# Optimization experiments

Measured on AMD Instinct MI355X. Metric: run time of the kernel, lower is better.

The kernel has to match this reference:

```python
import jax, jax.numpy as jnp
import numpy as np

BLOCK = 8
HALO = 3
HEADS = 8
DIM_HEAD = 64
DIM = 128
MAX_NEG = -3.402823466e38  # -torch.finfo(float32).max, matches the CUDA kernel


def _extract_patches(xp, nh, nw, block, K):
    # xp: [b, c, Hp, Wp] (already padded). Returns [b, c, nh, nw, K, K]
    ih = (jnp.arange(nh) * block)[:, None] + jnp.arange(K)[None, :]  # [nh, K]
    iw = (jnp.arange(nw) * block)[:, None] + jnp.arange(K)[None, :]  # [nw, K]
    return xp[..., ih[:, None, :, None], iw[None, :, None, :]]


def setup_inputs() -> dict:
    key = jax.random.key(0)
    k1, k2, k3, k4, k5 = jax.random.split(key, 5)
    inner = HEADS * DIM_HEAD
    x = jax.random.normal(k1, (4, DIM, 128, 128), dtype=jnp.float32)
    s = 1.0 / np.sqrt(DIM)
    Wq = jax.random.normal(k2, (DIM, inner), dtype=jnp.float32) * s
    Wkv = jax.random.normal(k3, (DIM, 2 * inner), dtype=jnp.float32) * s
    Wo = jax.random.normal(k4, (inner, DIM), dtype=jnp.float32) * (1.0 / np.sqrt(inner))
    bo = jax.random.normal(k5, (DIM,), dtype=jnp.float32) * 0.01
    return {"x": x, "Wq": Wq, "Wkv": Wkv, "Wo": Wo, "bo": bo}


def reference(x, Wq, Wkv, Wo, bo):
    b, c, h, w = x.shape
    block, halo, heads, dh = BLOCK, HALO, HEADS, DIM_HEAD
    K = block + 2 * halo
    nh, nw = h // block, w // block
    nb = nh * nw
    I, J = block * block, K * K
    scale = dh ** -0.5

    # queries per block: [b, nb, I, c]
    q_inp = (x.reshape(b, c, nh, block, nw, block)
              .transpose(0, 2, 4, 3, 5, 1)
              .reshape(b, nb, I, c))

    # halo key/value windows via unfold-equivalent patch extraction
    xp = jnp.pad(x, ((0, 0), (0, 0), (halo, halo), (halo, halo)))
    kv = _extract_patches(xp, nh, nw, block, K)           # [b, c, nh, nw, K, K]
    kv_inp = kv.transpose(0, 2, 3, 4, 5, 1).reshape(b, nb, J, c)

    # mask: True where the halo window overlaps padding
    ones = jnp.pad(jnp.ones((1, 1, h, w), x.dtype),
                   ((0, 0), (0, 0), (halo, halo), (halo, halo)))
    mask = (_extract_patches(ones, nh, nw, block, K).reshape(nb, J) == 0)

    q = (q_inp @ Wq).reshape(b, nb, I, heads, dh) * scale
    kvp = kv_inp @ Wkv                                    # [b, nb, J, 2*inner]
    inner = heads * dh
    k = kvp[..., :inner].reshape(b, nb, J, heads, dh)
    v = kvp[..., inner:].reshape(b, nb, J, heads, dh)

    sim = jnp.einsum('bnihd,bnjhd->bnhij', q, k)          # [b, nb, heads, I, J]
    sim = jnp.where(mask[None, :, None, None, :], MAX_NEG, sim)
    attn = jax.nn.softmax(sim, axis=-1)
    out = jnp.einsum('bnhij,bnjhd->bnihd', attn, v)       # [b, nb, I, heads, dh]

    out = out.reshape(b, nb, I, inner) @ Wo + bo          # [b, nb, I, c]
    out = (out.reshape(b, nh, nw, block, block, c)
              .transpose(0, 5, 1, 3, 2, 4)
              .reshape(b, c, h, w))
    return out
```

## Files before the change

kernel.cpp:

```cpp
#include <hip/hip_runtime.h>
#include <hip/hip_bf16.h>

typedef unsigned short ushort_t;
typedef __attribute__((ext_vector_type(8))) short short8;
typedef __attribute__((ext_vector_type(4))) short short4v;
typedef __attribute__((ext_vector_type(4))) float float4v;

__device__ __forceinline__ unsigned short f2b(float f) {
    unsigned int u = __float_as_uint(f);
    return (unsigned short)((u + 0x7fffu + ((u >> 16) & 1u)) >> 16);
}

#define MFMA(a, b, c) __builtin_amdgcn_mfma_f32_16x16x32_bf16((a), (b), (c), 0, 0, 0)

__global__ void prep_weights(const float* __restrict__ Wq,
                             const float* __restrict__ Wkv,
                             const float* __restrict__ Wo,
                             ushort_t* __restrict__ ws)
{
    int t = blockIdx.x * 256 + threadIdx.x;
    if (t < 65536) {
        int n = t >> 7, c = t & 127;
        ws[t] = f2b(Wq[c * 512 + n]);
    } else if (t < 196608) {
        int u = t - 65536;
        int h = u >> 14, r = (u >> 7) & 127, c = u & 127;
        float v = (r < 64) ? Wkv[c * 1024 + h * 64 + r]
                           : Wkv[c * 1024 + 512 + h * 64 + (r - 64)];
        ws[t] = f2b(v);
    } else {
        int u = t - 196608;
        int c = u >> 9, n = u & 511;
        ws[t] = f2b(Wo[n * 128 + c]);
    }
}

__global__ __launch_bounds__(512, 2)
void halo_attn_mfma(const float* __restrict__ xg,
                    const ushort_t* __restrict__ wqt,
                    const ushort_t* __restrict__ wkvt,
                    const ushort_t* __restrict__ wot,
                    const float* __restrict__ bo,
                    float* __restrict__ outg)
{
    extern __shared__ char smem[];
    ushort_t* s_x   = (ushort_t*)(smem);
    ushort_t* k_s   = (ushort_t*)(smem + 56576);
    ushort_t* v_t   = (ushort_t*)(smem + 86528);
    ushort_t* p_s   = (ushort_t*)(smem + 116224);
    ushort_t* q_s   = (ushort_t*)(smem + 145920);
    float*    s_max = (float*)(smem + 155136);
    float*    s_sum = (float*)(smem + 155648);
    ushort_t* o_s   = k_s;

    const int tid  = threadIdx.x;
    const int w    = tid >> 6;
    const int lane = tid & 63;
    const int m    = lane & 15;
    const int quad = lane >> 4;

    const int wg  = blockIdx.x;
    const int b   = wg >> 8;
    const int blk = wg & 255;
    const int by = blk >> 4, bx = blk & 15;
    const int y0 = by * 8 - 3, x0 = bx * 8 - 3;

    for (int t = tid; t < 64 * 24; t += 512) {
        int r = t / 24, c = 208 + (t - r * 24);
        p_s[r * 232 + c] = 0;
        v_t[r * 232 + c] = 0;
    }
    for (int t = tid; t < 128 * 256; t += 512) {
        int c = t >> 8, wy = (t >> 4) & 15, wx = t & 15;
        if (wy < 14 && wx < 14) {
            int gy = y0 + wy, gx = x0 + wx;
            float v = 0.f;
            if ((unsigned)gy < 128u && (unsigned)gx < 128u)
                v = xg[((b * 128 + c) * 128 + gy) * 128 + gx];
            s_x[(wy * 14 + wx) * 136 + c] = f2b(v);
        }
    }
    for (int t = tid; t < 12 * 128; t += 512)
        s_x[(196 + (t >> 7)) * 136 + (t & 127)] = 0;
    __syncthreads();

    float4v res[4];
#pragma unroll
    for (int i = 0; i < 4; ++i) res[i] = (float4v){0.f, 0.f, 0.f, 0.f};

    for (int h = 0; h < 8; ++h) {
        {
            const int nt = w & 7;
            const ushort_t* bb = wkvt + h * 16384 + (nt * 16 + m) * 128 + quad * 8;
            short8 bfr[4];
#pragma unroll
            for (int kk = 0; kk < 4; ++kk) bfr[kk] = *(const short8*)(bb + kk * 32);
#pragma unroll 1
            for (int jt = 0; jt < 13; ++jt) {
                float4v c = {0.f, 0.f, 0.f, 0.f};
                const ushort_t* ar = s_x + (jt * 16 + m) * 136 + quad * 8;
#pragma unroll
                for (int kk = 0; kk < 4; ++kk) {
                    short8 af = *(const short8*)(ar + kk * 32);
                    c = MFMA(af, bfr[kk], c);
                }
                if (nt < 4) {
                    int d = nt * 16 + m;
#pragma unroll
                    for (int r = 0; r < 4; ++r)
                        k_s[(jt * 16 + quad * 4 + r) * 72 + d] = f2b(c[r]);
                } else {
                    int dv = (nt - 4) * 16 + m;
                    short4v pk;
#pragma unroll
                    for (int r = 0; r < 4; ++r) pk[r] = (short)f2b(c[r]);
                    *(short4v*)(v_t + dv * 232 + jt * 16 + quad * 4) = pk;
                }
            }
        }
        {
            const int nt = w & 3;
            const ushort_t* bb = wqt + (h * 64 + nt * 16 + m) * 128 + quad * 8;
            short8 bfr[4];
#pragma unroll
            for (int kk = 0; kk < 4; ++kk) bfr[kk] = *(const short8*)(bb + kk * 32);
#pragma unroll
            for (int tt = 0; tt < 2; ++tt) {
                int it = (w >> 2) + tt * 2;
                float4v c = {0.f, 0.f, 0.f, 0.f};
                int i = it * 16 + m;
                int jq = ((i >> 3) + 3) * 14 + (i & 7) + 3;
                const ushort_t* ar = s_x + jq * 136 + quad * 8;
#pragma unroll
                for (int kk = 0; kk < 4; ++kk) {
                    short8 af = *(const short8*)(ar + kk * 32);
                    c = MFMA(af, bfr[kk], c);
                }
                int d = nt * 16 + m;
#pragma unroll
                for (int r = 0; r < 4; ++r)
                    q_s[(it * 16 + quad * 4 + r) * 72 + d] = f2b(c[r] * 0.125f);
            }
        }
        __syncthreads();

        {
            const int it = w & 3;
            const int half = w >> 2;
            const int jt0 = half ? 7 : 0;
            const int ntile = half ? 6 : 7;
            short8 aq[2];
#pragma unroll
            for (int kk = 0; kk < 2; ++kk)
                aq[kk] = *(const short8*)(q_s + (it * 16 + m) * 72 + kk * 32 + quad * 8);
            float sc[7][4];
            int okm = 0;
            float pm[4] = {-3.0e38f, -3.0e38f, -3.0e38f, -3.0e38f};
#pragma unroll
            for (int u = 0; u < 7; ++u) {
                if (u < ntile) {
                    int jt = jt0 + u;
                    float4v c = {0.f, 0.f, 0.f, 0.f};
#pragma unroll
                    for (int kk = 0; kk < 2; ++kk) {
                        short8 bk = *(const short8*)(k_s + (jt * 16 + m) * 72 + kk * 32 + quad * 8);
                        c = MFMA(aq[kk], bk, c);
                    }
                    int j = jt * 16 + m;
                    bool ok = false;
                    if (j < 196) {
                        int wy = j / 14, wx = j - wy * 14;
                        ok = ((unsigned)(y0 + wy) < 128u) && ((unsigned)(x0 + wx) < 128u);
                    }
                    if (ok) {
                        okm |= (1 << u);
#pragma unroll
                        for (int r = 0; r < 4; ++r) pm[r] = fmaxf(pm[r], c[r]);
                    }
#pragma unroll
                    for (int r = 0; r < 4; ++r) sc[u][r] = c[r];
                }
            }
#pragma unroll
            for (int mk = 1; mk < 16; mk <<= 1)
#pragma unroll
                for (int r = 0; r < 4; ++r)
                    pm[r] = fmaxf(pm[r], __shfl_xor(pm[r], mk, 64));
            if (m == 0) {
#pragma unroll
                for (int r = 0; r < 4; ++r)
                    s_max[half * 64 + it * 16 + quad * 4 + r] = pm[r];
            }
            __syncthreads();
            float m0[4], sm[4];
#pragma unroll
            for (int r = 0; r < 4; ++r) {
                int i = it * 16 + quad * 4 + r;
                m0[r] = fmaxf(s_max[i], s_max[64 + i]);
                sm[r] = 0.f;
            }
#pragma unroll
            for (int u = 0; u < 7; ++u) {
                if (u < ntile) {
                    int j = (jt0 + u) * 16 + m;
                    bool ok = (okm >> u) & 1;
#pragma unroll
                    for (int r = 0; r < 4; ++r) {
                        float p = ok ? __expf(sc[u][r] - m0[r]) : 0.f;
                        sm[r] += p;
                        p_s[(it * 16 + quad * 4 + r) * 232 + j] = f2b(p);
                    }
                }
            }
#pragma unroll
            for (int mk = 1; mk < 16; mk <<= 1)
#pragma unroll
                for (int r = 0; r < 4; ++r)
                    sm[r] += __shfl_xor(sm[r], mk, 64);
            if (m == 0) {
#pragma unroll
                for (int r = 0; r < 4; ++r)
                    s_sum[half * 64 + it * 16 + quad * 4 + r] = sm[r];
            }
            __syncthreads();
        }

        {
            const int nt = w & 3;
#pragma unroll
            for (int tt = 0; tt < 2; ++tt) {
                int it = (w >> 2) + tt * 2;
                float4v c = {0.f, 0.f, 0.f, 0.f};
                const ushort_t* ar = p_s + (it * 16 + m) * 232 + quad * 8;
                const ushort_t* br = v_t + (nt * 16 + m) * 232 + quad * 8;
#pragma unroll
                for (int kk = 0; kk < 7; ++kk) {
                    short8 af = *(const short8*)(ar + kk * 32);
                    short8 bf = *(const short8*)(br + kk * 32);
                    c = MFMA(af, bf, c);
                }
#pragma unroll
                for (int r = 0; r < 4; ++r) {
                    int i = it * 16 + quad * 4 + r;
                    float rv = 1.f / (s_sum[i] + s_sum[64 + i]);
                    o_s[i * 72 + nt * 16 + m] = f2b(c[r] * rv);
                }
            }
        }
        __syncthreads();

        {
            const int ct = w & 7;
            const ushort_t* bb = wot + (ct * 16 + m) * 512 + h * 64 + quad * 8;
            short8 bw[2];
#pragma unroll
            for (int kk = 0; kk < 2; ++kk) bw[kk] = *(const short8*)(bb + kk * 32);
#pragma unroll
            for (int it = 0; it < 4; ++it) {
                float4v c = res[it];
                const ushort_t* ar = o_s + (it * 16 + m) * 72 + quad * 8;
#pragma unroll
                for (int kk = 0; kk < 2; ++kk) {
                    short8 af = *(const short8*)(ar + kk * 32);
                    c = MFMA(af, bw[kk], c);
                }
                res[it] = c;
            }
        }
        __syncthreads();
    }

    {
        const int cch = (w & 7) * 16 + m;
        const float bias = bo[cch];
#pragma unroll
        for (int it = 0; it < 4; ++it) {
#pragma unroll
            for (int r = 0; r < 4; ++r) {
                int i = it * 16 + quad * 4 + r;
                int gy = by * 8 + (i >> 3), gx = bx * 8 + (i & 7);
                outg[((b * 128 + cch) * 128 + gy) * 128 + gx] = res[it][r] + bias;
            }
        }
    }
}

extern "C" void kernel_launch(void* const* d_in, const int* in_sizes, int n_in,
                              void* d_out, int out_size, void* d_ws, size_t ws_size,
                              hipStream_t stream) {
    const float* x   = (const float*)d_in[0];
    const float* Wq  = (const float*)d_in[1];
    const float* Wkv = (const float*)d_in[2];
    const float* Wo  = (const float*)d_in[3];
    const float* bo  = (const float*)d_in[4];
    float* out = (float*)d_out;
    ushort_t* ws = (ushort_t*)d_ws;

    prep_weights<<<dim3(1024), dim3(256), 0, stream>>>(Wq, Wkv, Wo, ws);

    (void)hipFuncSetAttribute((const void*)halo_attn_mfma,
                              hipFuncAttributeMaxDynamicSharedMemorySize, 156160);
    halo_attn_mfma<<<dim3(1024), dim3(512), 156160, stream>>>(
        x, ws, ws + 65536, ws + 196608, bo, out);
}
```

Before: 422.7 us.

## Swizzle LDS layouts, keep x fragments in registers, alias x buffer to shrink LDS

Replaces the padded LDS layouts with XOR-swizzled 16-byte chunk layouts for x, K, V, P, Q and O. The x window fragments for K/V and Q projections are now loaded once into registers, so the x buffer can alias K/V storage. This cuts dynamic shared memory from about 156KB to about 101KB. Each wave now loops over all 8 column tiles for its row tiles instead of one tile over all rows. It also vectorizes the x staging load into 8-channel packs. The aim is fewer bank conflicts and lower LDS pressure, at the cost of more registers held across the head loop.

```diff
diff --git a/kernel.cpp b/kernel.cpp
--- a/kernel.cpp
+++ b/kernel.cpp
@@ -44,14 +44,14 @@
                     float* __restrict__ outg)
 {
     extern __shared__ char smem[];
-    ushort_t* s_x   = (ushort_t*)(smem);
-    ushort_t* k_s   = (ushort_t*)(smem + 56576);
-    ushort_t* v_t   = (ushort_t*)(smem + 86528);
-    ushort_t* p_s   = (ushort_t*)(smem + 116224);
-    ushort_t* q_s   = (ushort_t*)(smem + 145920);
-    float*    s_max = (float*)(smem + 155136);
-    float*    s_sum = (float*)(smem + 155648);
-    ushort_t* o_s   = k_s;
+    ushort_t* k_u   = (ushort_t*)(smem);
+    ushort_t* v_u   = (ushort_t*)(smem + 26624);
+    ushort_t* sx_u  = (ushort_t*)(smem);
+    ushort_t* p_u   = (ushort_t*)(smem + 59392);
+    ushort_t* q_u   = (ushort_t*)(smem + 92160);
+    float*    s_max = (float*)(smem + 100352);
+    float*    s_sum = (float*)(smem + 100864);
+    ushort_t* o_u   = k_u;
 
     const int tid  = threadIdx.x;
     const int w    = tid >> 6;
@@ -65,81 +65,118 @@
     const int by = blk >> 4, bx = blk & 15;
     const int y0 = by * 8 - 3, x0 = bx * 8 - 3;
 
-    for (int t = tid; t < 64 * 24; t += 512) {
-        int r = t / 24, c = 208 + (t - r * 24);
-        p_s[r * 232 + c] = 0;
-        v_t[r * 232 + c] = 0;
-    }
-    for (int t = tid; t < 128 * 256; t += 512) {
-        int c = t >> 8, wy = (t >> 4) & 15, wx = t & 15;
-        if (wy < 14 && wx < 14) {
-            int gy = y0 + wy, gx = x0 + wx;
-            float v = 0.f;
-            if ((unsigned)gy < 128u && (unsigned)gx < 128u)
-                v = xg[((b * 128 + c) * 128 + gy) * 128 + gx];
-            s_x[(wy * 14 + wx) * 136 + c] = f2b(v);
-        }
-    }
-    for (int t = tid; t < 12 * 128; t += 512)
-        s_x[(196 + (t >> 7)) * 136 + (t & 127)] = 0;
+    const short8 zero8 = {0, 0, 0, 0, 0, 0, 0, 0};
+
+    for (int job = tid; job < 3136; job += 512) {
+        int cc  = job / 196;
+        int pos = job - cc * 196;
+        int wy = pos / 14;
+        int wx = pos - wy * 14;
+        int gy = y0 + wy, gx = x0 + wx;
+        short8 pk = zero8;
+        if ((unsigned)gy < 128u && (unsigned)gx < 128u) {
+            const float* xp = xg + ((b * 128 + cc * 8) * 128 + gy) * 128 + gx;
+#pragma unroll
+            for (int r = 0; r < 8; ++r)
+                pk[r] = (short)f2b(xp[r * 16384]);
+        }
+        *(short8*)(sx_u + pos * 128 + ((cc ^ (pos & 7)) << 3)) = pk;
+    }
+    for (int t = tid; t < 192; t += 512) {
+        int row = 196 + (t >> 4), cc = t & 15;
+        *(short8*)(sx_u + row * 128 + ((cc ^ (row & 7)) << 3)) = zero8;
+    }
     __syncthreads();
 
+    short8 xa[2][4];
+#pragma unroll
+    for (int u = 0; u < 2; ++u) {
+        int jt = w + 8 * u;
+#pragma unroll
+        for (int kk = 0; kk < 4; ++kk) {
+            xa[u][kk] = zero8;
+            if (jt < 13) {
+                int row = jt * 16 + m;
+                xa[u][kk] = *(const short8*)(sx_u + row * 128 +
+                                             (((kk * 4 + quad) ^ (m & 7)) << 3));
+            }
+        }
+    }
+    short8 qa[2][4];
+#pragma unroll
+    for (int tt = 0; tt < 2; ++tt) {
+        int it = (w >> 2) + 2 * tt;
+        int i  = it * 16 + m;
+        int jq = ((i >> 3) + 3) * 14 + (i & 7) + 3;
+#pragma unroll
+        for (int kk = 0; kk < 4; ++kk)
+            qa[tt][kk] = *(const short8*)(sx_u + jq * 128 +
+                                          (((kk * 4 + quad) ^ (jq & 7)) << 3));
+    }
+    __syncthreads();
+
+    for (int t = tid; t < 256; t += 512) {
+        int row = t >> 2, cc = 26 + (t & 1);
+        ushort_t* base = ((t >> 1) & 1) ? v_u : p_u;
+        *(short8*)(base + row * 256 + ((cc ^ (row & 7)) << 3)) = zero8;
+    }
+
     float4v res[4];
 #pragma unroll
     for (int i = 0; i < 4; ++i) res[i] = (float4v){0.f, 0.f, 0.f, 0.f};
 
     for (int h = 0; h < 8; ++h) {
-        {
-            const int nt = w & 7;
+#pragma unroll 1
+        for (int nt = 0; nt < 8; ++nt) {
             const ushort_t* bb = wkvt + h * 16384 + (nt * 16 + m) * 128 + quad * 8;
             short8 bfr[4];
 #pragma unroll
             for (int kk = 0; kk < 4; ++kk) bfr[kk] = *(const short8*)(bb + kk * 32);
-#pragma unroll 1
-            for (int jt = 0; jt < 13; ++jt) {
+#pragma unroll
+            for (int u = 0; u < 2; ++u) {
+                int jt = w + 8 * u;
+                if (jt < 13) {
+                    float4v c = {0.f, 0.f, 0.f, 0.f};
+#pragma unroll
+                    for (int kk = 0; kk < 4; ++kk) c = MFMA(xa[u][kk], bfr[kk], c);
+                    if (nt < 4) {
+                        int chunkx = nt * 2 + (m >> 3), inner = m & 7;
+#pragma unroll
+                        for (int r = 0; r < 4; ++r) {
+                            int row = jt * 16 + quad * 4 + r;
+                            k_u[row * 64 + ((chunkx ^ (row & 7)) << 3) + inner] = f2b(c[r]);
+                        }
+                    } else {
+                        int dv = (nt - 4) * 16 + m;
+                        int chunk = jt * 2 + (quad >> 1);
+                        short4v pk;
+#pragma unroll
+                        for (int r = 0; r < 4; ++r) pk[r] = (short)f2b(c[r]);
+                        *(short4v*)(v_u + dv * 256 + ((chunk ^ (dv & 7)) << 3) +
+                                    (quad & 1) * 4) = pk;
+                    }
+                }
+            }
+        }
+        {
+            const int ntq = w & 3;
+            const ushort_t* bb = wqt + (h * 64 + ntq * 16 + m) * 128 + quad * 8;
+            short8 bfr[4];
+#pragma unroll
+            for (int kk = 0; kk < 4; ++kk) bfr[kk] = *(const short8*)(bb + kk * 32);
+#pragma unroll
+            for (int tt = 0; tt < 2; ++tt) {
+                int it = (w >> 2) + 2 * tt;
                 float4v c = {0.f, 0.f, 0.f, 0.f};
-                const ushort_t* ar = s_x + (jt * 16 + m) * 136 + quad * 8;
-#pragma unroll
-                for (int kk = 0; kk < 4; ++kk) {
-                    short8 af = *(const short8*)(ar + kk * 32);
-                    c = MFMA(af, bfr[kk], c);
-                }
-                if (nt < 4) {
-                    int d = nt * 16 + m;
-#pragma unroll
-                    for (int r = 0; r < 4; ++r)
-                        k_s[(jt * 16 + quad * 4 + r) * 72 + d] = f2b(c[r]);
-                } else {
-                    int dv = (nt - 4) * 16 + m;
-                    short4v pk;
-#pragma unroll
-                    for (int r = 0; r < 4; ++r) pk[r] = (short)f2b(c[r]);
-                    *(short4v*)(v_t + dv * 232 + jt * 16 + quad * 4) = pk;
-                }
-            }
-        }
-        {
-            const int nt = w & 3;
-            const ushort_t* bb = wqt + (h * 64 + nt * 16 + m) * 128 + quad * 8;
-            short8 bfr[4];
-#pragma unroll
-            for (int kk = 0; kk < 4; ++kk) bfr[kk] = *(const short8*)(bb + kk * 32);
-#pragma unroll
-            for (int tt = 0; tt < 2; ++tt) {
-                int it = (w >> 2) + tt * 2;
-                float4v c = {0.f, 0.f, 0.f, 0.f};
-                int i = it * 16 + m;
-                int jq = ((i >> 3) + 3) * 14 + (i & 7) + 3;
-                const ushort_t* ar = s_x + jq * 136 + quad * 8;
-#pragma unroll
-                for (int kk = 0; kk < 4; ++kk) {
-                    short8 af = *(const short8*)(ar + kk * 32);
-                    c = MFMA(af, bfr[kk], c);
-                }
-                int d = nt * 16 + m;
-#pragma unroll
-                for (int r = 0; r < 4; ++r)
-                    q_s[(it * 16 + quad * 4 + r) * 72 + d] = f2b(c[r] * 0.125f);
+#pragma unroll
+                for (int kk = 0; kk < 4; ++kk) c = MFMA(qa[tt][kk], bfr[kk], c);
+                int chunkx = ntq * 2 + (m >> 3), inner = m & 7;
+#pragma unroll
+                for (int r = 0; r < 4; ++r) {
+                    int row = it * 16 + quad * 4 + r;
+                    q_u[row * 64 + ((chunkx ^ (row & 7)) << 3) + inner] =
+                        f2b(c[r] * 0.125f);
+                }
             }
         }
         __syncthreads();
@@ -152,7 +189,8 @@
             short8 aq[2];
 #pragma unroll
             for (int kk = 0; kk < 2; ++kk)
-                aq[kk] = *(const short8*)(q_s + (it * 16 + m) * 72 + kk * 32 + quad * 8);
+                aq[kk] = *(const short8*)(q_u + (it * 16 + m) * 64 +
+                                          (((kk * 4 + quad) ^ (m & 7)) << 3));
             float sc[7][4];
             int okm = 0;
             float pm[4] = {-3.0e38f, -3.0e38f, -3.0e38f, -3.0e38f};
@@ -163,7 +201,8 @@
                     float4v c = {0.f, 0.f, 0.f, 0.f};
 #pragma unroll
                     for (int kk = 0; kk < 2; ++kk) {
-                        short8 bk = *(const short8*)(k_s + (jt * 16 + m) * 72 + kk * 32 + quad * 8);
+                        short8 bk = *(const short8*)(k_u + (jt * 16 + m) * 64 +
+                                                     (((kk * 4 + quad) ^ (m & 7)) << 3));
                         c = MFMA(aq[kk], bk, c);
                     }
                     int j = jt * 16 + m;
@@ -203,12 +242,14 @@
             for (int u = 0; u < 7; ++u) {
                 if (u < ntile) {
                     int j = (jt0 + u) * 16 + m;
+                    int chunk = (j >> 3);
                     bool ok = (okm >> u) & 1;
 #pragma unroll
                     for (int r = 0; r < 4; ++r) {
+                        int i = it * 16 + quad * 4 + r;
                         float p = ok ? __expf(sc[u][r] - m0[r]) : 0.f;
                         sm[r] += p;
-                        p_s[(it * 16 + quad * 4 + r) * 232 + j] = f2b(p);
+                        p_u[i * 256 + ((chunk ^ (i & 7)) << 3) + (j & 7)] = f2b(p);
                     }
                 }
             }
@@ -229,21 +270,22 @@
             const int nt = w & 3;
 #pragma unroll
             for (int tt = 0; tt < 2; ++tt) {
-                int it = (w >> 2) + tt * 2;
+                int it = (w >> 2) + 2 * tt;
                 float4v c = {0.f, 0.f, 0.f, 0.f};
-                const ushort_t* ar = p_s + (it * 16 + m) * 232 + quad * 8;
-                const ushort_t* br = v_t + (nt * 16 + m) * 232 + quad * 8;
 #pragma unroll
                 for (int kk = 0; kk < 7; ++kk) {
-                    short8 af = *(const short8*)(ar + kk * 32);
-                    short8 bf = *(const short8*)(br + kk * 32);
+                    short8 af = *(const short8*)(p_u + (it * 16 + m) * 256 +
+                                                 (((kk * 4 + quad) ^ (m & 7)) << 3));
+                    short8 bf = *(const short8*)(v_u + (nt * 16 + m) * 256 +
+                                                 (((kk * 4 + quad) ^ (m & 7)) << 3));
                     c = MFMA(af, bf, c);
                 }
+                int chunkx = nt * 2 + (m >> 3), inner = m & 7;
 #pragma unroll
                 for (int r = 0; r < 4; ++r) {
                     int i = it * 16 + quad * 4 + r;
                     float rv = 1.f / (s_sum[i] + s_sum[64 + i]);
-                    o_s[i * 72 + nt * 16 + m] = f2b(c[r] * rv);
+                    o_u[i * 64 + ((chunkx ^ (i & 7)) << 3) + inner] = f2b(c[r] * rv);
                 }
             }
         }
@@ -258,10 +300,10 @@
 #pragma unroll
             for (int it = 0; it < 4; ++it) {
                 float4v c = res[it];
-                const ushort_t* ar = o_s + (it * 16 + m) * 72 + quad * 8;
 #pragma unroll
                 for (int kk = 0; kk < 2; ++kk) {
-                    short8 af = *(const short8*)(ar + kk * 32);
+                    short8 af = *(const short8*)(o_u + (it * 16 + m) * 64 +
+                                                 (((kk * 4 + quad) ^ (m & 7)) << 3));
                     c = MFMA(af, bw[kk], c);
                 }
                 res[it] = c;
@@ -299,7 +341,7 @@
     prep_weights<<<dim3(1024), dim3(256), 0, stream>>>(Wq, Wkv, Wo, ws);
 
     (void)hipFuncSetAttribute((const void*)halo_attn_mfma,
-                              hipFuncAttributeMaxDynamicSharedMemorySize, 156160);
-    halo_attn_mfma<<<dim3(1024), dim3(512), 156160, stream>>>(
+                              hipFuncAttributeMaxDynamicSharedMemorySize, 101376);
+    halo_attn_mfma<<<dim3(1024), dim3(512), 101376, stream>>>(
         x, ws, ws + 65536, ws + 196608, bo, out);
 }
```

After: 507.6 us. 1.2x slower.
